# Kernel tuning notes

Measured on AMD Instinct MI355X. Metric: run time of the kernel, lower is better.

Reference implementation:

```python
import jax, jax.numpy as jnp
import numpy as np

NF = 96   # out_channel_M
G = 8     # deformable groups
K = 3     # deform conv kernel size


def conv2d(x, w, b, stride=1, pad=1):
    out = jax.lax.conv_general_dilated(x, w, (stride, stride), [(pad, pad), (pad, pad)],
                                       dimension_numbers=('NCHW', 'OIHW', 'NCHW'))
    return out + b[None, :, None, None]


def conv_transpose2d(x, w, b, stride=2, pad=1, out_pad=1):
    # PyTorch ConvTranspose2d semantics; w is [Cin, Cout, k, k]
    k = w.shape[2]
    wt = jnp.flip(w, (2, 3)).transpose(1, 0, 2, 3)  # -> OIHW
    p = (k - 1 - pad, k - 1 - pad + out_pad)
    out = jax.lax.conv_general_dilated(x, wt, (1, 1), [p, p], lhs_dilation=(stride, stride),
                                       dimension_numbers=('NCHW', 'OIHW', 'NCHW'))
    return out + b[None, :, None, None]


def lrelu(x):
    return jax.nn.leaky_relu(x, 0.1)


def deform_conv(x, offset, w, b):
    """DCNv1: offset-driven bilinear sampling + 3x3 contraction (stride=1, pad=1).
    x: [B,C,H,W], offset: [B, 2*G*K*K, H, W] (per-group (dy,dx) interleaved per tap)."""
    B, C, H, W = x.shape
    K2 = K * K
    Cg = C // G
    off = offset.reshape(B, G, K2, 2, H, W)
    ky, kx = jnp.meshgrid(jnp.arange(K), jnp.arange(K), indexing='ij')
    # sampling positions: p = p0 + p_k + delta_p  (zero padding of 1)
    py = (jnp.arange(H, dtype=x.dtype)[None, None, None, :, None]
          + (ky.reshape(K2) - 1).astype(x.dtype)[None, None, :, None, None] + off[:, :, :, 0])
    px = (jnp.arange(W, dtype=x.dtype)[None, None, None, None, :]
          + (kx.reshape(K2) - 1).astype(x.dtype)[None, None, :, None, None] + off[:, :, :, 1])
    y0 = jnp.floor(py); x0 = jnp.floor(px)
    ly = py - y0; lx = px - x0
    y0i = y0.astype(jnp.int32); x0i = x0.astype(jnp.int32)
    xg = x.reshape(B, G, Cg, H * W)  # channels within a deformable group share offsets

    def gather(yi, xi):
        valid = ((yi >= 0) & (yi < H) & (xi >= 0) & (xi < W)).astype(x.dtype)  # [B,G,K2,H,W]
        idx = jnp.clip(yi, 0, H - 1) * W + jnp.clip(xi, 0, W - 1)
        g = jnp.take_along_axis(xg, idx.reshape(B, G, 1, K2 * H * W), axis=3)
        return g.reshape(B, G, Cg, K2, H, W) * valid[:, :, None]

    bw = lambda a: a[:, :, None]  # broadcast bilinear weight over channel axis
    v = (gather(y0i, x0i) * bw((1 - ly) * (1 - lx))
         + gather(y0i, x0i + 1) * bw((1 - ly) * lx)
         + gather(y0i + 1, x0i) * bw(ly * (1 - lx))
         + gather(y0i + 1, x0i + 1) * bw(ly * lx))
    sampled = v.reshape(B, C, K2, H, W)
    out = jnp.einsum('bckhw,ock->bohw', sampled, w.reshape(w.shape[0], C, K2))
    return out + b[None, :, None, None]


def setup_inputs():
    key = jax.random.key(0)
    ks = jax.random.split(key, 16)
    B, H, W = 2, 128, 128
    s = 0.05
    wgt = lambda k, shape: jax.random.normal(k, shape, jnp.float32) * s
    return {
        'ref_fea': jax.random.normal(ks[0], (B, NF, H, W), jnp.float32),
        'inp_fea': jax.random.normal(ks[1], (B, NF, H, W), jnp.float32),
        'oc1_w': wgt(ks[2], (NF, 2 * NF, 3, 3)), 'oc1_b': jnp.zeros((NF,), jnp.float32),
        'oc3_w': wgt(ks[3], (NF, NF, 3, 3)), 'oc3_b': jnp.zeros((NF,), jnp.float32),
        'enc1_w': wgt(ks[4], (NF, NF, 3, 3)), 'enc1_b': jnp.zeros((NF,), jnp.float32),
        'enc2_w': wgt(ks[5], (NF, NF, 3, 3)), 'enc2_b': jnp.zeros((NF,), jnp.float32),
        'dec1_w': wgt(ks[6], (NF, NF, 3, 3)), 'dec1_b': jnp.zeros((NF,), jnp.float32),
        'dec2_w': wgt(ks[7], (NF, NF, 3, 3)), 'dec2_b': jnp.zeros((NF,), jnp.float32),
        'coff_w': wgt(ks[8], (2 * G * K * K, NF, 3, 3)), 'coff_b': jnp.zeros((2 * G * K * K,), jnp.float32),
        'dcn_w': wgt(ks[9], (NF, NF, 3, 3)), 'dcn_b': jnp.zeros((NF,), jnp.float32),
        'ref1_w': wgt(ks[10], (NF, 2 * NF, 3, 3)), 'ref1_b': jnp.zeros((NF,), jnp.float32),
        'ref2_w': wgt(ks[11], (NF, NF, 3, 3)), 'ref2_b': jnp.zeros((NF,), jnp.float32),
    }


def reference(ref_fea, inp_fea, oc1_w, oc1_b, oc3_w, oc3_b, enc1_w, enc1_b, enc2_w, enc2_b,
              dec1_w, dec1_b, dec2_w, dec2_b, coff_w, coff_b, dcn_w, dcn_b,
              ref1_w, ref1_b, ref2_w, ref2_b):
    # MotionEstimation
    t = jnp.concatenate([ref_fea, inp_fea], axis=1)
    t = lrelu(conv2d(t, oc1_w, oc1_b))
    t = lrelu(conv2d(t, oc3_w, oc3_b))
    en_offset = conv2d(lrelu(conv2d(t, enc1_w, enc1_b, stride=2)), enc2_w, enc2_b, stride=2)
    # Q: round-to-integer quantization (straight-through; same forward value as round)
    q_offset = en_offset + jax.lax.stop_gradient(jnp.round(en_offset) - en_offset)
    # MotionCompensation
    de_offset = conv_transpose2d(lrelu(conv_transpose2d(q_offset, dec1_w, dec1_b)), dec2_w, dec2_b)
    offset = conv2d(de_offset, coff_w, coff_b)  # conv_offset inside DCNv1 (extra_offset_mask)
    aligned = deform_conv(ref_fea, offset, dcn_w, dcn_b)
    r = lrelu(conv2d(jnp.concatenate([aligned, ref_fea], axis=1), ref1_w, ref1_b))
    r = lrelu(conv2d(r, ref2_w, ref2_b))
    return aligned + r, en_offset, q_offset
```

## Files before the change

kernel.cpp:

```cpp
#include <hip/hip_runtime.h>
#include <hip/hip_bf16.h>

typedef __hip_bfloat16 bf16;
typedef __attribute__((ext_vector_type(8))) short s8;
typedef __attribute__((ext_vector_type(4))) short s4;
typedef __attribute__((ext_vector_type(4))) float f4;

#define N_FEA   3145728
#define N_EN    196608
#define N_E1    786432
#define OUT_EN  3145728
#define OUT_Q   3342336

__device__ __forceinline__ float b2f(bf16 v) { return __bfloat162float(v); }
__device__ __forceinline__ float bs2f(short v) {
    union { unsigned u; float f; } x; x.u = ((unsigned)(unsigned short)v) << 16; return x.f;
}

__global__ void wpack_sw(const float* __restrict__ w1, const float* __restrict__ w3,
                         float* __restrict__ o1, float* __restrict__ o3) {
    long i = (long)blockIdx.x * 256 + threadIdx.x;
    const long n1 = 2L * 12 * 96 * 72;
    if (i < n1) {
        int ky = (int)(i % 3); long t = i / 3;
        int o = (int)(t % 8); t /= 8;
        int kx = (int)(t % 3); t /= 3;
        int c = (int)(t % 96); t /= 96;
        int ocg = (int)(t % 12); int ks = (int)(t / 12);
        o1[i] = w1[((long)(ocg * 8 + o) * 192 + ks * 96 + c) * 9 + ky * 3 + kx];
        return;
    }
    i -= n1;
    const long n3 = 2L * 12 * 48 * 72;
    if (i < n3) {
        int ky = (int)(i % 3); long t = i / 3;
        int o = (int)(t % 8); t /= 8;
        int kx = (int)(t % 3); t /= 3;
        int c = (int)(t % 48); t /= 48;
        int ocg = (int)(t % 12); int ks = (int)(t / 12);
        o3[i] = w3[((long)(ocg * 8 + o) * 96 + ks * 48 + c) * 9 + ky * 3 + kx];
    }
}

__global__ void wpack_enc(const float* __restrict__ w1, const float* __restrict__ w2,
                          float* __restrict__ o1, float* __restrict__ o2) {
    long i = (long)blockIdx.x * 256 + threadIdx.x;
    const long n1 = 24L * 96 * 4 * 9;
    if (i < n1) {
        int k = (int)(i % 9);
        int o = (int)((i / 9) % 4);
        int c = (int)((i / 36) % 96);
        int ocg = (int)(i / (36 * 96));
        o1[i] = w1[((long)(ocg * 4 + o) * 96 + c) * 9 + k];
        return;
    }
    i -= n1;
    const long n2 = 48L * 96 * 2 * 9;
    if (i < n2) {
        int k = (int)(i % 9);
        int o = (int)((i / 9) % 2);
        int c = (int)((i / 18) % 96);
        int ocg = (int)(i / (18 * 96));
        o2[i] = w2[((long)(ocg * 2 + o) * 96 + c) * 9 + k];
    }
}

__global__ void wpack_dec(const float* __restrict__ w1, const float* __restrict__ w2,
                          float* __restrict__ o1, float* __restrict__ o2) {
    long i = (long)blockIdx.x * 256 + threadIdx.x;
    const long n1 = 48L * 96 * 2 * 9;
    if (i < n1) {
        int k = (int)(i % 9);
        int o = (int)((i / 9) % 2);
        int c = (int)((i / 18) % 96);
        int ocg = (int)(i / (18 * 96));
        o1[i] = w1[((long)c * 96 + ocg * 2 + o) * 9 + k];
        return;
    }
    i -= n1;
    const long n2 = 24L * 96 * 4 * 9;
    if (i < n2) {
        int k = (int)(i % 9);
        int o = (int)((i / 9) % 4);
        int c = (int)((i / 36) % 96);
        int ocg = (int)(i / (36 * 96));
        o2[i] = w2[((long)c * 96 + ocg * 4 + o) * 9 + k];
    }
}

template <int OCB>
__global__ __launch_bounds__(256) void conv3x3_sw(
    const float* __restrict__ inA, int cA, int bstrA,
    const float* __restrict__ inB, int cB, int bstrB,
    const float* __restrict__ wsc,
    float* __restrict__ P0, float* __restrict__ P1, int Cout) {
    const int H = 128, W = 128;
    const int NOC = Cout / OCB;
    int bid = blockIdx.x;
    const int ks = bid & 1;
    int r = bid >> 1;
    const int strip = r & 31; r >>= 5;
    const int ocg = r % NOC;
    const int b = r / NOC;
    const float* in = ks ? inB : inA;
    const int cN = ks ? cB : cA;
    const int bstr = ks ? bstrB : bstrA;
    float* P = ks ? P1 : P0;
    const float* wq0 = wsc + ((long)(ks * NOC + ocg) * cN) * 72;

    const int sr = strip >> 1, cp = strip & 1;
    const int ox = cp * 64 + (threadIdx.x & 63);
    const int rg = threadIdx.x >> 6;
    const int oy0 = sr * 8 + rg * 2;
    const int iyb = oy0 - 1;

    bool vy[4];
#pragma unroll
    for (int j = 0; j < 4; ++j) vy[j] = (unsigned)(iyb + j) < (unsigned)H;

    float acc[OCB][2];
#pragma unroll
    for (int o = 0; o < OCB; ++o)
#pragma unroll
        for (int j = 0; j < 2; ++j) acc[o][j] = 0.f;

    const float* pc = in + (long)b * bstr * H * W + (long)iyb * W;
    for (int c = 0; c < cN; ++c) {
        const float* wq = wq0 + c * 72;
#pragma unroll
        for (int kx = 0; kx < 3; ++kx) {
            const int ix = ox + kx - 1;
            const bool vx = (unsigned)ix < (unsigned)W;
            float rv[4];
#pragma unroll
            for (int j = 0; j < 4; ++j)
                rv[j] = (vx && vy[j]) ? pc[j * W + ix] : 0.f;
#pragma unroll
            for (int o = 0; o < OCB; ++o) {
#pragma unroll
                for (int ky = 0; ky < 3; ++ky) {
                    float wz = wq[kx * 24 + o * 3 + ky];
#pragma unroll
                    for (int j = 0; j < 2; ++j)
                        acc[o][j] = fmaf(rv[j + ky], wz, acc[o][j]);
                }
            }
        }
        pc += (long)H * W;
    }
#pragma unroll
    for (int o = 0; o < OCB; ++o) {
        long base = (((long)b * Cout + ocg * OCB + o) * H + oy0) * W + ox;
        P[base] = acc[o][0];
        P[base + W] = acc[o][1];
    }
}

__global__ void fuse_add_k(const float* __restrict__ p0, const float* __restrict__ p1,
                           const float* __restrict__ bias, float* __restrict__ out) {
    long idx = (long)blockIdx.x * 256 + threadIdx.x;
    if (idx >= (long)N_FEA) return;
    int oc = (int)((idx >> 14) % 96);
    float a = bias[oc] + p0[idx] + p1[idx];
    out[idx] = a > 0.f ? a : 0.1f * a;
}

template <int OCB>
__global__ __launch_bounds__(256) void conv_s2_px(
    const float* __restrict__ in, int Cin, int Hin, int Win,
    const float* __restrict__ wsc, const float* __restrict__ bias,
    float* __restrict__ out, int Cout, int relu,
    float* __restrict__ qq, float* __restrict__ qf2) {
    const int Hout = Hin >> 1, Wout = Win >> 1;
    const int rpb = 256 / Wout;
    const int strips = Hout / rpb;
    int bid = blockIdx.x;
    const int strip = bid % strips; bid /= strips;
    const int NOC = Cout / OCB;
    const int ocg = bid % NOC;
    const int b = bid / NOC;
    const int tid = threadIdx.x;
    const int ox = tid % Wout;
    const int oy = strip * rpb + tid / Wout;
    const int iy0 = oy * 2 - 1, ix0 = ox * 2 - 1;
    const float* wq0 = wsc + (long)(ocg * Cin) * (OCB * 9);

    float acc[OCB];
#pragma unroll
    for (int o = 0; o < OCB; ++o) acc[o] = bias[ocg * OCB + o];
    const bool vx0 = ix0 >= 0;
    const bool vy0 = iy0 >= 0;

    const float* pc = in + (long)b * Cin * Hin * Win + (long)iy0 * Win + ix0;
    for (int c = 0; c < Cin; ++c) {
        float rv[3][3];
#pragma unroll
        for (int jr = 0; jr < 3; ++jr) {
            const float* row = pc + jr * Win;
            const bool vr = jr ? true : vy0;
            rv[jr][0] = (vr && vx0) ? row[0] : 0.f;
            rv[jr][1] = vr ? row[1] : 0.f;
            rv[jr][2] = vr ? row[2] : 0.f;
        }
        const float* wq = wq0 + c * (OCB * 9);
#pragma unroll
        for (int o = 0; o < OCB; ++o)
#pragma unroll
            for (int ky = 0; ky < 3; ++ky)
#pragma unroll
                for (int kx = 0; kx < 3; ++kx)
                    acc[o] = fmaf(rv[ky][kx], wq[o * 9 + ky * 3 + kx], acc[o]);
        pc += (long)Hin * Win;
    }
#pragma unroll
    for (int o = 0; o < OCB; ++o) {
        long idx = (((long)b * Cout + ocg * OCB + o) * Hout + oy) * Wout + ox;
        float a = acc[o];
        if (relu) a = a > 0.f ? a : 0.1f * a;
        out[idx] = a;
        if (qq) {
            float qv = rintf(a);
            qq[idx] = qv;
            qf2[idx] = qv;
        }
    }
}

template <int OCB, int HWC>
__global__ __launch_bounds__(256) void convt_quad(
    const float* __restrict__ in, const float* __restrict__ wsc,
    const float* __restrict__ bias, void* __restrict__ out,
    int Hin, int Win, int relu) {
    const int C = 96;
    const int Hout = 2 * Hin, Wout = 2 * Win;
    const int strips = (Hin * Win) / 256;
    int bid = blockIdx.x;
    const int strip = bid % strips; bid /= strips;
    const int NOC = C / OCB;
    const int ocg = bid % NOC;
    const int b = bid / NOC;
    const int idx = strip * 256 + threadIdx.x;
    const int iy = idx / Win, ix = idx % Win;
    const bool vr = (ix + 1) < Win, vd = (iy + 1) < Hin;
    const float* wq0 = wsc + (long)(ocg * C) * (OCB * 9);

    float acc[OCB][4];
#pragma unroll
    for (int o = 0; o < OCB; ++o) {
        float bz = bias[ocg * OCB + o];
#pragma unroll
        for (int j = 0; j < 4; ++j) acc[o][j] = bz;
    }
    const float* pc = in + (long)b * C * Hin * Win + (long)iy * Win + ix;
    for (int c = 0; c < C; ++c) {
        float i00 = pc[0];
        float i01 = vr ? pc[1] : 0.f;
        float i10 = vd ? pc[Win] : 0.f;
        float i11 = (vr && vd) ? pc[Win + 1] : 0.f;
        const float* wq = wq0 + c * (OCB * 9);
#pragma unroll
        for (int o = 0; o < OCB; ++o) {
            const float* w = wq + o * 9;
            acc[o][0] = fmaf(i00, w[4], acc[o][0]);
            acc[o][1] = fmaf(i01, w[3], fmaf(i00, w[5], acc[o][1]));
            acc[o][2] = fmaf(i10, w[1], fmaf(i00, w[7], acc[o][2]));
            acc[o][3] = fmaf(i11, w[0],
                        fmaf(i10, w[2],
                        fmaf(i01, w[6],
                        fmaf(i00, w[8], acc[o][3]))));
        }
        pc += (long)Hin * Win;
    }
#pragma unroll
    for (int o = 0; o < OCB; ++o) {
        int oc = ocg * OCB + o;
#pragma unroll
        for (int j = 0; j < 4; ++j) {
            float a = acc[o][j];
            if (relu) a = a > 0.f ? a : 0.1f * a;
            int oy = 2 * iy + (j >> 1), ox2 = 2 * ix + (j & 1);
            if (HWC)
                ((bf16*)out)[((long)b * Hout * Wout + (long)oy * Wout + ox2) * 96 + oc] =
                    __float2bfloat16(a);
            else
                ((float*)out)[(((long)b * C + oc) * Hout + oy) * Wout + ox2] = a;
        }
    }
}

__device__ __forceinline__ void packw(const float* __restrict__ w, bf16* __restrict__ wP,
                                      int Cin, int swap, long i) {
    const int cpt = Cin >> 5;
    int e = (int)(i & 7);
    int n16 = (int)((i >> 3) & 15);
    int q = (int)((i >> 7) & 3);
    long t = i >> 9;
    int ci = (int)(t % cpt); t /= cpt;
    int tap = (int)(t % 9);
    int g = (int)(t / 9);
    int oc = g * 16 + n16;
    int c = ci * 32 + q * 8 + e;
    int cs = swap ? (c + Cin / 2) % Cin : c;
    wP[i] = __float2bfloat16(w[((long)oc * Cin + cs) * 9 + tap]);
}
__global__ void wxform_all(const float* __restrict__ coffw, const float* __restrict__ ref1w,
                           const float* __restrict__ ref2w, const float* __restrict__ dcnw,
                           bf16* __restrict__ p_coff, bf16* __restrict__ p_ref1,
                           bf16* __restrict__ p_ref2, bf16* __restrict__ p_dcn) {
    const long n1 = 124416, n2 = 165888, n3 = 82944, n4 = 82944;
    long i = (long)blockIdx.x * 256 + threadIdx.x;
    if (i < n1) { packw(coffw, p_coff, 96, 0, i); return; }
    i -= n1;
    if (i < n2) { packw(ref1w, p_ref1, 192, 1, i); return; }
    i -= n2;
    if (i < n3) { packw(ref2w, p_ref2, 96, 0, i); return; }
    i -= n3;
    if (i < n4) {
        int e = (int)(i & 7);
        int n16 = (int)((i >> 3) & 15);
        int q = (int)((i >> 7) & 3);
        long t = i >> 9;
        int ci = (int)(t % 27);
        int g = (int)(t / 27);
        int kp = ci * 32 + q * 8 + e;
        int c = kp % 96, kk = kp / 96;
        p_dcn[i] = __float2bfloat16(dcnw[(long)(g * 16 + n16) * 864 + c * 9 + kk]);
    }
}

__global__ void pack_hwc(const float* __restrict__ src, bf16* __restrict__ dst,
                         int HW, int Cs, int coff) {
    long i = (long)blockIdx.x * 256 + threadIdx.x;
    if (i >= 2L * 96 * HW) return;
    int px = (int)(i % HW);
    long t = i / HW;
    int c = (int)(t % 96);
    int b = (int)(t / 96);
    dst[((long)b * HW + px) * Cs + coff + c] = __float2bfloat16(src[i]);
}

template <int EPI>
__global__ __launch_bounds__(256) void mconv(
    const bf16* __restrict__ X, const bf16* __restrict__ wP,
    const float* __restrict__ bias, void* __restrict__ out,
    const bf16* __restrict__ res,
    int Cin, int Cout, int H, int W, int relu) {
    const int HW = H * W;
    const int NG = Cout >> 4, split = (NG + 1) >> 1;
    int bid = blockIdx.x;
    const int nb = HW >> 6;
    const int pxb = (bid % nb) << 6;
    const int b = bid / nb;
    const int wave = threadIdx.x >> 6, lane = threadIdx.x & 63;
    const int mt = (wave >> 1) << 5;
    const int og0 = (wave & 1) ? split : 0;
    const int og1 = (wave & 1) ? NG : split;
    const int q = lane >> 4, n16 = lane & 15;
    const int pA0 = pxb + mt + n16, pA1 = pA0 + 16;
    const int oy0 = pA0 / W, ox0 = pA0 % W;
    const int oy1 = pA1 / W, ox1 = pA1 % W;
    const long ib = (long)b * HW * Cin;
    f4 acc0[5], acc1[5];
    const f4 z4 = {0.f, 0.f, 0.f, 0.f};
#pragma unroll
    for (int g = 0; g < 5; ++g) { acc0[g] = z4; acc1[g] = z4; }
    const s8 z8 = {0, 0, 0, 0, 0, 0, 0, 0};
    const int cpt = Cin >> 5;
    const int lofs = lane << 3;
    for (int tap = 0; tap < 9; ++tap) {
        const int ky = tap / 3 - 1, kx = tap % 3 - 1;
        const int iy0 = oy0 + ky, ix0 = ox0 + kx;
        const int iy1 = oy1 + ky, ix1 = ox1 + kx;
        const bool v0 = (unsigned)iy0 < (unsigned)H && (unsigned)ix0 < (unsigned)W;
        const bool v1 = (unsigned)iy1 < (unsigned)H && (unsigned)ix1 < (unsigned)W;
        const bf16* pa0 = X + ib + ((long)iy0 * W + ix0) * Cin + q * 8;
        const bf16* pa1 = X + ib + ((long)iy1 * W + ix1) * Cin + q * 8;
        for (int ci = 0; ci < cpt; ++ci) {
            const int c0 = ci << 5;
            s8 a0 = v0 ? *(const s8*)(pa0 + c0) : z8;
            s8 a1 = v1 ? *(const s8*)(pa1 + c0) : z8;
#pragma unroll
            for (int gi = 0; gi < 5; ++gi) {
                int g = og0 + gi;
                if (g >= og1) break;
                s8 bb = *(const s8*)(wP + ((long)(g * 9 + tap) * cpt + ci) * 512 + lofs);
                acc0[gi] = __builtin_amdgcn_mfma_f32_16x16x32_bf16(a0, bb, acc0[gi], 0, 0, 0);
                acc1[gi] = __builtin_amdgcn_mfma_f32_16x16x32_bf16(a1, bb, acc1[gi], 0, 0, 0);
            }
        }
    }
#pragma unroll
    for (int gi = 0; gi < 5; ++gi) {
        int g = og0 + gi;
        if (g >= og1) break;
        int oc = g * 16 + n16;
        float bz = bias[oc];
#pragma unroll
        for (int t = 0; t < 2; ++t) {
            f4 a = t ? acc1[gi] : acc0[gi];
            int pxl = pxb + mt + t * 16 + q * 4;
#pragma unroll
            for (int r = 0; r < 4; ++r) {
                float v = a[r] + bz;
                if (relu) v = v > 0.f ? v : 0.1f * v;
                int px = pxl + r;
                if (EPI == 0)
                    ((bf16*)out)[((long)b * HW + px) * Cout + oc] = __float2bfloat16(v);
                else {
                    v += b2f(res[((long)b * HW + px) * 192 + 96 + oc]);
                    ((float*)out)[((long)b * Cout + oc) * HW + px] = v;
                }
            }
        }
    }
}

__global__ __launch_bounds__(256, 4) void deform_m_k(
    const bf16* __restrict__ Xref, const bf16* __restrict__ offs,
    const bf16* __restrict__ wD, const float* __restrict__ db,
    bf16* __restrict__ X2) {
    const int H = 128, W = 128;
    __shared__ bf16 offL[16 * 144];
    __shared__ bf16 s[16][872];
    int bid = blockIdx.x;
    const int band = bid & 7;
    int r = bid >> 3;
    const int b = r >> 7; r &= 127;
    const int rowin = r >> 3, xb = r & 7;
    const int oy = band * 16 + rowin;
    const int ox0 = xb * 16;
    const int tid = threadIdx.x;
    const long pxbase = (long)b * (H * W) + oy * W + ox0;
    for (int e = tid; e < 16 * 144; e += 256)
        offL[e] = offs[(pxbase + (e / 144)) * 144 + (e % 144)];
    __syncthreads();
    const long refb = (long)b * (H * W);
    for (int e = tid; e < 16 * 72; e += 256) {
        int p = e / 72, rem = e % 72;
        int g8 = rem / 9, kk = rem % 9;
        int ox = ox0 + p;
        float offy = b2f(offL[p * 144 + g8 * 18 + kk * 2]);
        float offx = b2f(offL[p * 144 + g8 * 18 + kk * 2 + 1]);
        float py = (float)(oy + kk / 3 - 1) + offy;
        float px = (float)(ox + kk % 3 - 1) + offx;
        float y0f = floorf(py), x0f = floorf(px);
        float ly = py - y0f, lx = px - x0f;
        int y0 = (int)y0f, x0 = (int)x0f;
        float w00 = (1.f - ly) * (1.f - lx), w01 = (1.f - ly) * lx;
        float w10 = ly * (1.f - lx), w11 = ly * lx;
        float v[12];
#pragma unroll
        for (int j = 0; j < 12; ++j) v[j] = 0.f;
        auto corner = [&](int yy, int xx, float wgt) {
            if ((unsigned)yy < (unsigned)H && (unsigned)xx < (unsigned)W) {
                const s4* cp = (const s4*)(Xref + (refb + yy * W + xx) * 192 + g8 * 12);
                s4 c0 = cp[0], c1 = cp[1], c2 = cp[2];
#pragma unroll
                for (int j = 0; j < 4; ++j) {
                    v[j]     = fmaf(bs2f(c0[j]), wgt, v[j]);
                    v[4 + j] = fmaf(bs2f(c1[j]), wgt, v[4 + j]);
                    v[8 + j] = fmaf(bs2f(c2[j]), wgt, v[8 + j]);
                }
            }
        };
        corner(y0, x0, w00);
        corner(y0, x0 + 1, w01);
        corner(y0 + 1, x0, w10);
        corner(y0 + 1, x0 + 1, w11);
        short rr[12];
#pragma unroll
        for (int j = 0; j < 12; ++j) {
            bf16 h = __float2bfloat16(v[j]);
            rr[j] = *(short*)&h;
        }
        s4* dst = (s4*)&s[p][kk * 96 + g8 * 12];
        dst[0] = ((s4*)rr)[0];
        dst[1] = ((s4*)rr)[1];
        dst[2] = ((s4*)rr)[2];
    }
    __syncthreads();
    const int wave = tid >> 6, lane = tid & 63;
    const int q = lane >> 4, n16 = lane & 15;
    const f4 z4 = {0.f, 0.f, 0.f, 0.f};
    for (int g = wave; g < 6; g += 4) {
        f4 acc = z4;
        const bf16* wg = wD + (long)g * 27 * 512 + (lane << 3);
#pragma unroll 3
        for (int ci = 0; ci < 27; ++ci) {
            s8 a = *(const s8*)&s[n16][ci * 32 + q * 8];
            s8 bb = *(const s8*)(wg + ci * 512);
            acc = __builtin_amdgcn_mfma_f32_16x16x32_bf16(a, bb, acc, 0, 0, 0);
        }
        int oc = g * 16 + n16;
        float bz = db[oc];
#pragma unroll
        for (int rr2 = 0; rr2 < 4; ++rr2) {
            int p = q * 4 + rr2;
            X2[(pxbase + p) * 192 + 96 + oc] = __float2bfloat16(acc[rr2] + bz);
        }
    }
}

extern "C" void kernel_launch(void* const* d_in, const int* in_sizes, int n_in,
                              void* d_out, int out_size, void* d_ws, size_t ws_size,
                              hipStream_t stream) {
    const float* ref_fea = (const float*)d_in[0];
    const float* inp_fea = (const float*)d_in[1];
    const float* oc1_w = (const float*)d_in[2];  const float* oc1_b = (const float*)d_in[3];
    const float* oc3_w = (const float*)d_in[4];  const float* oc3_b = (const float*)d_in[5];
    const float* enc1_w = (const float*)d_in[6]; const float* enc1_b = (const float*)d_in[7];
    const float* enc2_w = (const float*)d_in[8]; const float* enc2_b = (const float*)d_in[9];
    const float* dec1_w = (const float*)d_in[10]; const float* dec1_b = (const float*)d_in[11];
    const float* dec2_w = (const float*)d_in[12]; const float* dec2_b = (const float*)d_in[13];
    const float* coff_w = (const float*)d_in[14]; const float* coff_b = (const float*)d_in[15];
    const float* dcn_w = (const float*)d_in[16];  const float* dcn_b = (const float*)d_in[17];
    const float* ref1_w = (const float*)d_in[18]; const float* ref1_b = (const float*)d_in[19];
    const float* ref2_w = (const float*)d_in[20]; const float* ref2_b = (const float*)d_in[21];

    float* out = (float*)d_out;
    float* OUTS = out;
    float* S1 = (float*)d_ws;
    float* S2 = S1 + N_FEA;
    float* F = S1 + N_E1;
    bf16* de_hwc = (bf16*)S1;
    bf16* offs = (bf16*)S2;
    bf16* X2 = (bf16*)S1;
    bf16* r1 = (bf16*)S2;
    bf16* wtb = (bf16*)S2 + 4800000;
    bf16* wt_coff = wtb;
    bf16* wt_ref1 = wt_coff + 124416;
    bf16* wt_ref2 = wt_ref1 + 165888;
    bf16* wt_dcn = wt_ref2 + 82944;
    float* wdec1 = (float*)(wt_dcn + 82944);
    float* wdec2 = wdec1 + 82944;
    float* wsc1 = out + OUT_EN;
    float* wsc3 = wsc1 + 165888;
    float* wenc1 = S1 + 1048576;
    float* wenc2 = wenc1 + 82944;

    dim3 blk(256);
    auto nb = [](long n) { return dim3((unsigned)((n + 255) / 256)); };

    wpack_sw<<<nb(165888L + 82944), blk, 0, stream>>>(oc1_w, oc3_w, wsc1, wsc3);
    conv3x3_sw<8><<<dim3(1536), blk, 0, stream>>>(ref_fea, 96, 96,
                                                  inp_fea, 96, 96,
                                                  wsc1, S1, S2, 96);
    fuse_add_k<<<nb(N_FEA), blk, 0, stream>>>(S1, S2, oc1_b, OUTS);
    conv3x3_sw<8><<<dim3(1536), blk, 0, stream>>>(OUTS, 48, 96,
                                                  OUTS + 48 * 16384, 48, 96,
                                                  wsc3, S1, S2, 96);
    fuse_add_k<<<nb(N_FEA), blk, 0, stream>>>(S1, S2, oc3_b, OUTS);
    wpack_enc<<<nb(82944L + 82944), blk, 0, stream>>>(enc1_w, enc2_w, wenc1, wenc2);
    conv_s2_px<4><<<dim3(768), blk, 0, stream>>>(OUTS, 96, 128, 128,
                                                 wenc1, enc1_b, S1, 96, 1,
                                                 nullptr, nullptr);
    wxform_all<<<nb(124416L + 165888 + 82944 + 82944), blk, 0, stream>>>(
        coff_w, ref1_w, ref2_w, dcn_w, wt_coff, wt_ref1, wt_ref2, wt_dcn);
    wpack_dec<<<nb(82944L + 82944), blk, 0, stream>>>(dec1_w, dec2_w, wdec1, wdec2);
    conv_s2_px<2><<<dim3(384), blk, 0, stream>>>(S1, 96, 64, 64,
                                                 wenc2, enc2_b, out + OUT_EN, 96, 0,
                                                 out + OUT_Q, F);
    convt_quad<2, 0><<<dim3(384), blk, 0, stream>>>(F, wdec1, dec1_b, S2, 32, 32, 1);
    convt_quad<4, 1><<<dim3(768), blk, 0, stream>>>(S2, wdec2, dec2_b, de_hwc, 64, 64, 0);
    mconv<0><<<dim3(512), blk, 0, stream>>>(de_hwc, wt_coff, coff_b, offs, nullptr,
                                            96, 144, 128, 128, 0);
    pack_hwc<<<nb(N_FEA), blk, 0, stream>>>(ref_fea, X2, 16384, 192, 0);
    deform_m_k<<<dim3(2048), blk, 0, stream>>>(X2, offs, wt_dcn, dcn_b, X2);
    mconv<0><<<dim3(512), blk, 0, stream>>>(X2, wt_ref1, ref1_b, r1, nullptr,
                                            192, 96, 128, 128, 1);
    mconv<3><<<dim3(512), blk, 0, stream>>>(r1, wt_ref2, ref2_b, out, X2,
                                            96, 96, 128, 128, 1);
}
```

Measured before the change: 776.5 us.

## Fuse split-K conv halves with bias/lrelu epilogue; widen mconv blocks to 8 waves

```diff
diff --git a/kernel.cpp b/kernel.cpp
--- a/kernel.cpp
+++ b/kernel.cpp
@@ -89,80 +89,99 @@
 }
 
 template <int OCB>
-__global__ __launch_bounds__(256) void conv3x3_sw(
-    const float* __restrict__ inA, int cA, int bstrA,
-    const float* __restrict__ inB, int cB, int bstrB,
-    const float* __restrict__ wsc,
-    float* __restrict__ P0, float* __restrict__ P1, int Cout) {
+__global__ __launch_bounds__(256) void conv3x3_fu(
+    const float* __restrict__ in0, int c0, int bstr0,
+    const float* __restrict__ in1, int c1, int bstr1,
+    const float* __restrict__ wsc, const float* __restrict__ bias,
+    float* __restrict__ outp, int Cout) {
     const int H = 128, W = 128;
     const int NOC = Cout / OCB;
     int bid = blockIdx.x;
-    const int ks = bid & 1;
-    int r = bid >> 1;
-    const int strip = r & 31; r >>= 5;
-    const int ocg = r % NOC;
-    const int b = r / NOC;
-    const float* in = ks ? inB : inA;
-    const int cN = ks ? cB : cA;
-    const int bstr = ks ? bstrB : bstrA;
-    float* P = ks ? P1 : P0;
-    const float* wq0 = wsc + ((long)(ks * NOC + ocg) * cN) * 72;
-
-    const int sr = strip >> 1, cp = strip & 1;
-    const int ox = cp * 64 + (threadIdx.x & 63);
+    const int pan = bid & 1; bid >>= 1;
+    const int strip = bid & 15; bid >>= 4;
+    const int ocg = bid % NOC;
+    const int b = bid / NOC;
+
+    const int ox = pan * 64 + (threadIdx.x & 63);
     const int rg = threadIdx.x >> 6;
-    const int oy0 = sr * 8 + rg * 2;
+    const int oy0 = strip * 8 + rg * 2;
     const int iyb = oy0 - 1;
 
     bool vy[4];
 #pragma unroll
     for (int j = 0; j < 4; ++j) vy[j] = (unsigned)(iyb + j) < (unsigned)H;
 
-    float acc[OCB][2];
+    float accA[OCB][2], accB[OCB][2];
 #pragma unroll
     for (int o = 0; o < OCB; ++o)
 #pragma unroll
-        for (int j = 0; j < 2; ++j) acc[o][j] = 0.f;
-
-    const float* pc = in + (long)b * bstr * H * W + (long)iyb * W;
-    for (int c = 0; c < cN; ++c) {
-        const float* wq = wq0 + c * 72;
-#pragma unroll
-        for (int kx = 0; kx < 3; ++kx) {
-            const int ix = ox + kx - 1;
-            const bool vx = (unsigned)ix < (unsigned)W;
-            float rv[4];
-#pragma unroll
-            for (int j = 0; j < 4; ++j)
-                rv[j] = (vx && vy[j]) ? pc[j * W + ix] : 0.f;
-#pragma unroll
-            for (int o = 0; o < OCB; ++o) {
-#pragma unroll
-                for (int ky = 0; ky < 3; ++ky) {
-                    float wz = wq[kx * 24 + o * 3 + ky];
-#pragma unroll
-                    for (int j = 0; j < 2; ++j)
-                        acc[o][j] = fmaf(rv[j + ky], wz, acc[o][j]);
+        for (int j = 0; j < 2; ++j) { accA[o][j] = 0.f; accB[o][j] = 0.f; }
+
+    {
+        const float* wq0 = wsc + (long)ocg * c0 * 72;
+        const float* pc = in0 + (long)b * bstr0 * H * W + (long)iyb * W;
+        for (int c = 0; c < c0; ++c) {
+            const float* wq = wq0 + c * 72;
+#pragma unroll
+            for (int kx = 0; kx < 3; ++kx) {
+                const int ix = ox + kx - 1;
+                const bool vx = (unsigned)ix < (unsigned)W;
+                float rv[4];
+#pragma unroll
+                for (int j = 0; j < 4; ++j)
+                    rv[j] = (vx && vy[j]) ? pc[j * W + ix] : 0.f;
+#pragma unroll
+                for (int o = 0; o < OCB; ++o) {
+#pragma unroll
+                    for (int ky = 0; ky < 3; ++ky) {
+                        float wz = wq[kx * 24 + o * 3 + ky];
+#pragma unroll
+                        for (int j = 0; j < 2; ++j)
+                            accA[o][j] = fmaf(rv[j + ky], wz, accA[o][j]);
+                    }
                 }
             }
-        }
-        pc += (long)H * W;
+            pc += (long)H * W;
+        }
+    }
+    {
+        const float* wq0 = wsc + ((long)NOC + ocg) * c1 * 72;
+        const float* pc = in1 + (long)b * bstr1 * H * W + (long)iyb * W;
+        for (int c = 0; c < c1; ++c) {
+            const float* wq = wq0 + c * 72;
+#pragma unroll
+            for (int kx = 0; kx < 3; ++kx) {
+                const int ix = ox + kx - 1;
+                const bool vx = (unsigned)ix < (unsigned)W;
+                float rv[4];
+#pragma unroll
+                for (int j = 0; j < 4; ++j)
+                    rv[j] = (vx && vy[j]) ? pc[j * W + ix] : 0.f;
+#pragma unroll
+                for (int o = 0; o < OCB; ++o) {
+#pragma unroll
+                    for (int ky = 0; ky < 3; ++ky) {
+                        float wz = wq[kx * 24 + o * 3 + ky];
+#pragma unroll
+                        for (int j = 0; j < 2; ++j)
+                            accB[o][j] = fmaf(rv[j + ky], wz, accB[o][j]);
+                    }
+                }
+            }
+            pc += (long)H * W;
+        }
     }
 #pragma unroll
     for (int o = 0; o < OCB; ++o) {
+        float bz = bias[ocg * OCB + o];
         long base = (((long)b * Cout + ocg * OCB + o) * H + oy0) * W + ox;
-        P[base] = acc[o][0];
-        P[base + W] = acc[o][1];
-    }
-}
-
-__global__ void fuse_add_k(const float* __restrict__ p0, const float* __restrict__ p1,
-                           const float* __restrict__ bias, float* __restrict__ out) {
-    long idx = (long)blockIdx.x * 256 + threadIdx.x;
-    if (idx >= (long)N_FEA) return;
-    int oc = (int)((idx >> 14) % 96);
-    float a = bias[oc] + p0[idx] + p1[idx];
-    out[idx] = a > 0.f ? a : 0.1f * a;
+#pragma unroll
+        for (int j = 0; j < 2; ++j) {
+            float a = (bz + accA[o][j]) + accB[o][j];
+            a = a > 0.f ? a : 0.1f * a;
+            outp[base + (long)j * W] = a;
+        }
+    }
 }
 
 template <int OCB>
@@ -340,7 +359,7 @@
 }
 
 template <int EPI>
-__global__ __launch_bounds__(256) void mconv(
+__global__ __launch_bounds__(512) void mconv(
     const bf16* __restrict__ X, const bf16* __restrict__ wP,
     const float* __restrict__ bias, void* __restrict__ out,
     const bf16* __restrict__ res,
@@ -352,40 +371,33 @@
     const int pxb = (bid % nb) << 6;
     const int b = bid / nb;
     const int wave = threadIdx.x >> 6, lane = threadIdx.x & 63;
-    const int mt = (wave >> 1) << 5;
-    const int og0 = (wave & 1) ? split : 0;
-    const int og1 = (wave & 1) ? NG : split;
+    const int mq = wave & 3;
+    const int og0 = (wave >> 2) ? split : 0;
+    const int og1 = (wave >> 2) ? NG : split;
     const int q = lane >> 4, n16 = lane & 15;
-    const int pA0 = pxb + mt + n16, pA1 = pA0 + 16;
-    const int oy0 = pA0 / W, ox0 = pA0 % W;
-    const int oy1 = pA1 / W, ox1 = pA1 % W;
+    const int pA = pxb + mq * 16 + n16;
+    const int oyA = pA / W, oxA = pA % W;
     const long ib = (long)b * HW * Cin;
-    f4 acc0[5], acc1[5];
+    f4 acc[5];
     const f4 z4 = {0.f, 0.f, 0.f, 0.f};
 #pragma unroll
-    for (int g = 0; g < 5; ++g) { acc0[g] = z4; acc1[g] = z4; }
+    for (int g = 0; g < 5; ++g) acc[g] = z4;
     const s8 z8 = {0, 0, 0, 0, 0, 0, 0, 0};
     const int cpt = Cin >> 5;
     const int lofs = lane << 3;
     for (int tap = 0; tap < 9; ++tap) {
         const int ky = tap / 3 - 1, kx = tap % 3 - 1;
-        const int iy0 = oy0 + ky, ix0 = ox0 + kx;
-        const int iy1 = oy1 + ky, ix1 = ox1 + kx;
-        const bool v0 = (unsigned)iy0 < (unsigned)H && (unsigned)ix0 < (unsigned)W;
-        const bool v1 = (unsigned)iy1 < (unsigned)H && (unsigned)ix1 < (unsigned)W;
-        const bf16* pa0 = X + ib + ((long)iy0 * W + ix0) * Cin + q * 8;
-        const bf16* pa1 = X + ib + ((long)iy1 * W + ix1) * Cin + q * 8;
+        const int iy = oyA + ky, ix = oxA + kx;
+        const bool v = (unsigned)iy < (unsigned)H && (unsigned)ix < (unsigned)W;
+        const bf16* pa = X + ib + ((long)iy * W + ix) * Cin + q * 8;
         for (int ci = 0; ci < cpt; ++ci) {
-            const int c0 = ci << 5;
-            s8 a0 = v0 ? *(const s8*)(pa0 + c0) : z8;
-            s8 a1 = v1 ? *(const s8*)(pa1 + c0) : z8;
+            s8 a = v ? *(const s8*)(pa + (ci << 5)) : z8;
 #pragma unroll
             for (int gi = 0; gi < 5; ++gi) {
                 int g = og0 + gi;
                 if (g >= og1) break;
                 s8 bb = *(const s8*)(wP + ((long)(g * 9 + tap) * cpt + ci) * 512 + lofs);
-                acc0[gi] = __builtin_amdgcn_mfma_f32_16x16x32_bf16(a0, bb, acc0[gi], 0, 0, 0);
-                acc1[gi] = __builtin_amdgcn_mfma_f32_16x16x32_bf16(a1, bb, acc1[gi], 0, 0, 0);
+                acc[gi] = __builtin_amdgcn_mfma_f32_16x16x32_bf16(a, bb, acc[gi], 0, 0, 0);
             }
         }
     }
@@ -395,21 +407,17 @@
         if (g >= og1) break;
         int oc = g * 16 + n16;
         float bz = bias[oc];
-#pragma unroll
-        for (int t = 0; t < 2; ++t) {
-            f4 a = t ? acc1[gi] : acc0[gi];
-            int pxl = pxb + mt + t * 16 + q * 4;
-#pragma unroll
-            for (int r = 0; r < 4; ++r) {
-                float v = a[r] + bz;
-                if (relu) v = v > 0.f ? v : 0.1f * v;
-                int px = pxl + r;
-                if (EPI == 0)
-                    ((bf16*)out)[((long)b * HW + px) * Cout + oc] = __float2bfloat16(v);
-                else {
-                    v += b2f(res[((long)b * HW + px) * 192 + 96 + oc]);
-                    ((float*)out)[((long)b * Cout + oc) * HW + px] = v;
-                }
+        int pxl = pxb + mq * 16 + q * 4;
+#pragma unroll
+        for (int r = 0; r < 4; ++r) {
+            float v = acc[gi][r] + bz;
+            if (relu) v = v > 0.f ? v : 0.1f * v;
+            int px = pxl + r;
+            if (EPI == 0)
+                ((bf16*)out)[((long)b * HW + px) * Cout + oc] = __float2bfloat16(v);
+            else {
+                v += b2f(res[((long)b * HW + px) * 192 + 96 + oc]);
+                ((float*)out)[((long)b * Cout + oc) * HW + px] = v;
             }
         }
     }
@@ -521,6 +529,7 @@
     float* OUTS = out;
     float* S1 = (float*)d_ws;
     float* S2 = S1 + N_FEA;
+    float* T2 = S2;
     float* F = S1 + N_E1;
     bf16* de_hwc = (bf16*)S1;
     bf16* offs = (bf16*)S2;
@@ -542,16 +551,14 @@
     auto nb = [](long n) { return dim3((unsigned)((n + 255) / 256)); };
 
     wpack_sw<<<nb(165888L + 82944), blk, 0, stream>>>(oc1_w, oc3_w, wsc1, wsc3);
-    conv3x3_sw<8><<<dim3(1536), blk, 0, stream>>>(ref_fea, 96, 96,
-                                                  inp_fea, 96, 96,
-                                                  wsc1, S1, S2, 96);
-    fuse_add_k<<<nb(N_FEA), blk, 0, stream>>>(S1, S2, oc1_b, OUTS);
-    conv3x3_sw<8><<<dim3(1536), blk, 0, stream>>>(OUTS, 48, 96,
-                                                  OUTS + 48 * 16384, 48, 96,
-                                                  wsc3, S1, S2, 96);
-    fuse_add_k<<<nb(N_FEA), blk, 0, stream>>>(S1, S2, oc3_b, OUTS);
+    conv3x3_fu<8><<<dim3(768), blk, 0, stream>>>(ref_fea, 96, 96,
+                                                 inp_fea, 96, 96,
+                                                 wsc1, oc1_b, OUTS, 96);
+    conv3x3_fu<8><<<dim3(768), blk, 0, stream>>>(OUTS, 48, 96,
+                                                 OUTS + 48 * 16384, 48, 96,
+                                                 wsc3, oc3_b, T2, 96);
     wpack_enc<<<nb(82944L + 82944), blk, 0, stream>>>(enc1_w, enc2_w, wenc1, wenc2);
-    conv_s2_px<4><<<dim3(768), blk, 0, stream>>>(OUTS, 96, 128, 128,
+    conv_s2_px<4><<<dim3(768), blk, 0, stream>>>(T2, 96, 128, 128,
                                                  wenc1, enc1_b, S1, 96, 1,
                                                  nullptr, nullptr);
     wxform_all<<<nb(124416L + 165888 + 82944 + 82944), blk, 0, stream>>>(
@@ -562,12 +569,12 @@
                                                  out + OUT_Q, F);
     convt_quad<2, 0><<<dim3(384), blk, 0, stream>>>(F, wdec1, dec1_b, S2, 32, 32, 1);
     convt_quad<4, 1><<<dim3(768), blk, 0, stream>>>(S2, wdec2, dec2_b, de_hwc, 64, 64, 0);
-    mconv<0><<<dim3(512), blk, 0, stream>>>(de_hwc, wt_coff, coff_b, offs, nullptr,
-                                            96, 144, 128, 128, 0);
+    mconv<0><<<dim3(512), dim3(512), 0, stream>>>(de_hwc, wt_coff, coff_b, offs, nullptr,
+                                                  96, 144, 128, 128, 0);
     pack_hwc<<<nb(N_FEA), blk, 0, stream>>>(ref_fea, X2, 16384, 192, 0);
     deform_m_k<<<dim3(2048), blk, 0, stream>>>(X2, offs, wt_dcn, dcn_b, X2);
-    mconv<0><<<dim3(512), blk, 0, stream>>>(X2, wt_ref1, ref1_b, r1, nullptr,
-                                            192, 96, 128, 128, 1);
-    mconv<3><<<dim3(512), blk, 0, stream>>>(r1, wt_ref2, ref2_b, out, X2,
-                                            96, 96, 128, 128, 1);
-}
+    mconv<0><<<dim3(512), dim3(512), 0, stream>>>(X2, wt_ref1, ref1_b, r1, nullptr,
+                                                  192, 96, 128, 128, 1);
+    mconv<3><<<dim3(512), dim3(512), 0, stream>>>(r1, wt_ref2, ref2_b, out, X2,
+                                                  96, 96, 128, 128, 1);
+}
```

New measurement: 819.2 us. 1.05x slower.
